# Optimization experiments

Measured on AMD Instinct MI355X. Metric: run time of the kernel, lower is better.

Reference implementation:

```python
import jax, jax.numpy as jnp
import numpy as np

B, T, C = 8, 2048, 1024   # batch, seq_len, n_embd
H = 128                   # head_size

def setup_inputs() -> dict:
    key = jax.random.key(0)
    kx, kk, kq, kv = jax.random.split(key, 4)
    scale = 1.0 / np.sqrt(C)
    return {
        "x": jax.random.normal(kx, (B, T, C), dtype=jnp.float32),
        "Wk": jax.random.normal(kk, (C, H), dtype=jnp.float32) * scale,
        "Wq": jax.random.normal(kq, (C, H), dtype=jnp.float32) * scale,
        "Wv": jax.random.normal(kv, (C, H), dtype=jnp.float32) * scale,
    }

def reference(x, Wk, Wq, Wv):
    # k,q,v: [B,T,H]
    k = x @ Wk
    q = x @ Wq
    v = x @ Wv
    # NOTE: original scales by C**-0.5 (n_embd), not head_size**-0.5
    wei = jnp.einsum("bth,bsh->bts", q, k) * (x.shape[-1] ** -0.5)  # [B,T,T]
    wei = jax.nn.softmax(wei, axis=-1)  # no causal mask in the source module
    # dropout = 0.0 -> identity
    out = jnp.einsum("bts,bsh->bth", wei, v)  # [B,T,H]
    return out
```

## Files before the change

kernel.cpp:

```cpp
#include <hip/hip_runtime.h>
#include <hip/hip_bf16.h>
#include <stdint.h>
#include <stddef.h>

#define NB 8
#define NT 2048
#define NC 1024
#define NH 128

typedef float f32x4 __attribute__((ext_vector_type(4)));
typedef short bf16x8 __attribute__((ext_vector_type(8)));

__device__ __forceinline__ unsigned short f2bf(float f) {
    union { float f; uint32_t u; } v; v.f = f;
    uint32_t u = v.u;
    u += 0x7fffu + ((u >> 16) & 1u);
    return (unsigned short)(u >> 16);
}

__device__ __forceinline__ void gld16(const void* gp, void* lp) {
    __builtin_amdgcn_global_load_lds(
        (const __attribute__((address_space(1))) unsigned int*)gp,
        (__attribute__((address_space(3))) unsigned int*)lp, 16, 0, 0);
}


__global__ __launch_bounds__(256) void cast_w_kernel(const float* __restrict__ Wq,
                                                     const float* __restrict__ Wk,
                                                     const float* __restrict__ Wv,
                                                     unsigned short* __restrict__ Wtf) {
    int gid  = blockIdx.x * 256 + threadIdx.x;
    int lane = gid & 63;
    int fs   = gid >> 6;
    int kb   = fs & 31;
    int g    = fs >> 5;
    int w    = g >> 3;
    int g16  = g & 7;
    int quad = lane >> 4;
    int l16  = lane & 15;
    const float* src = (w == 0) ? Wq : ((w == 1) ? Wk : Wv);
    int n = g16 * 16 + l16;
    bf16x8 o;
#pragma unroll
    for (int j = 0; j < 8; ++j)
        o[j] = (short)f2bf(src[(size_t)(kb * 32 + quad * 8 + j) * 128 + n]);
    *(bf16x8*)(Wtf + (size_t)gid * 8) = o;
}

#define CS2 392

__global__ __launch_bounds__(512, 2) void proj_kernel(const float* __restrict__ x,
                                                      const unsigned short* __restrict__ Wtf,
                                                      unsigned short* __restrict__ Qf,
                                                      unsigned short* __restrict__ Kf,
                                                      unsigned short* __restrict__ Vf) {
    __shared__ __align__(16) unsigned short wbuf[4][24 * 512];

    const int tid  = threadIdx.x;
    const int wave = tid >> 6;
    const int lane = tid & 63;
    const int quad = lane >> 4;
    const int l16  = lane & 15;
    const int bidx = blockIdx.x;
    const int rowbase = bidx * 64;
    const int b    = bidx >> 5;
    const int mh   = wave & 1;
    const int nq   = wave >> 1;

    const float* xr0 = x + (size_t)(rowbase + mh * 32 + l16) * NC;
    const float* xr1 = xr0 + (size_t)16 * NC;

    float4 aS[2][4];
    f32x4 acc0[6] = {};
    f32x4 acc1[6] = {};

#define STAGE(KB, BI) { _Pragma("unroll") \
    for (int i_ = 0; i_ < 3; ++i_) { \
        const int g_ = wave * 3 + i_; \
        gld16(Wtf + ((size_t)(g_ * 32 + (KB)) * 512) + lane * 8, &wbuf[BI][g_ * 512]); } }

#define LOADA(KB, S) { \
    const float* p0_ = xr0 + (KB) * 32 + quad * 8; \
    aS[S][0] = *(const float4*)p0_; \
    aS[S][1] = *(const float4*)(p0_ + 4); \
    const float* p1_ = xr1 + (KB) * 32 + quad * 8; \
    aS[S][2] = *(const float4*)p1_; \
    aS[S][3] = *(const float4*)(p1_ + 4); }

#define BARW(N) { asm volatile("s_waitcnt vmcnt(" #N ") lgkmcnt(0)" ::: "memory"); \
                  __builtin_amdgcn_s_barrier(); }

#define ITER(K, CUR, SLOT, DOA, DOST) { \
    bf16x8 af0, af1; \
    af0[0] = (short)f2bf(aS[SLOT][0].x); af0[1] = (short)f2bf(aS[SLOT][0].y); \
    af0[2] = (short)f2bf(aS[SLOT][0].z); af0[3] = (short)f2bf(aS[SLOT][0].w); \
    af0[4] = (short)f2bf(aS[SLOT][1].x); af0[5] = (short)f2bf(aS[SLOT][1].y); \
    af0[6] = (short)f2bf(aS[SLOT][1].z); af0[7] = (short)f2bf(aS[SLOT][1].w); \
    af1[0] = (short)f2bf(aS[SLOT][2].x); af1[1] = (short)f2bf(aS[SLOT][2].y); \
    af1[2] = (short)f2bf(aS[SLOT][2].z); af1[3] = (short)f2bf(aS[SLOT][2].w); \
    af1[4] = (short)f2bf(aS[SLOT][3].x); af1[5] = (short)f2bf(aS[SLOT][3].y); \
    af1[6] = (short)f2bf(aS[SLOT][3].z); af1[7] = (short)f2bf(aS[SLOT][3].w); \
    if (DOA)  LOADA((K) + 2, SLOT); \
    if (DOST) STAGE((K) + 3, ((K) + 3) & 3); \
    _Pragma("unroll") \
    for (int i_ = 0; i_ < 6; ++i_) { \
        bf16x8 wf_ = *(const bf16x8*)(&wbuf[CUR][(nq * 6 + i_) * 512 + lane * 8]); \
        acc0[i_] = __builtin_amdgcn_mfma_f32_16x16x32_bf16(af0, wf_, acc0[i_], 0, 0, 0); \
        acc1[i_] = __builtin_amdgcn_mfma_f32_16x16x32_bf16(af1, wf_, acc1[i_], 0, 0, 0); } }

    LOADA(0, 0); LOADA(1, 1);
    STAGE(0, 0); STAGE(1, 1); STAGE(2, 2);
    BARW(6);

    for (int kb4 = 0; kb4 < 28; kb4 += 4) {
        ITER(kb4 + 0, 0, 0, 1, 1); BARW(14);
        ITER(kb4 + 1, 1, 1, 1, 1); BARW(14);
        ITER(kb4 + 2, 2, 0, 1, 1); BARW(14);
        ITER(kb4 + 3, 3, 1, 1, 1); BARW(14);
    }
    ITER(28, 0, 0, 1, 1); BARW(14);
    ITER(29, 1, 1, 1, 0); BARW(11);
    ITER(30, 2, 0, 0, 0); BARW(4);
    ITER(31, 3, 1, 0, 0);
    asm volatile("s_waitcnt vmcnt(0) lgkmcnt(0)" ::: "memory");
    __builtin_amdgcn_s_barrier();

    unsigned short* cs = (unsigned short*)wbuf;
#pragma unroll
    for (int i = 0; i < 6; ++i) {
#pragma unroll
        for (int r = 0; r < 4; ++r) {
            cs[(mh * 32 +  0 + quad * 4 + r) * CS2 + nq * 96 + i * 16 + l16] = f2bf(acc0[i][r]);
            cs[(mh * 32 + 16 + quad * 4 + r) * CS2 + nq * 96 + i * 16 + l16] = f2bf(acc1[i][r]);
        }
    }
    __syncthreads();

    const int ibase = (rowbase & (NT - 1)) >> 4;
    const int tc    = (rowbase & (NT - 1)) >> 5;
    unsigned short* qdst = Qf + (size_t)b * (NT * NH);
    unsigned short* kdst = Kf + (size_t)b * (NT * NH);
    unsigned short* vdst = Vf + (size_t)b * (NT * NH);

#pragma unroll
    for (int j = 0; j < 6; ++j) {
        const int s = wave * 6 + j;
        if (s < 32) {
            const int isK = s >> 4;
            const int t   = s & 15;
            const int m   = t >> 2;
            const int ks  = t & 3;
            unsigned short* dst = isK ? kdst : qdst;
            bf16x8 v = *(const bf16x8*)(&cs[(m * 16 + l16) * CS2 + isK * 128 + ks * 32 + quad * 8]);
            *(bf16x8*)(dst + ((size_t)((ibase + m) * 4 + ks) * 64 + lane) * 8) = v;
        } else {
            const int vv = s - 32;
            const int nt = vv >> 1;
            const int cc = vv & 1;
            bf16x8 v;
#pragma unroll
            for (int jj = 0; jj < 8; ++jj)
                v[jj] = (short)cs[(cc * 32 + quad * 8 + jj) * CS2 + 256 + nt * 16 + l16];
            *(bf16x8*)(vdst + ((size_t)(nt * 64 + tc + cc) * 64 + lane) * 8) = v;
        }
    }

#undef ITER
#undef BARW
#undef LOADA
#undef STAGE
}

__global__ __launch_bounds__(256, 2) void attn_kernel(const unsigned short* __restrict__ Qf,
                                                      const unsigned short* __restrict__ Kf,
                                                      const unsigned short* __restrict__ Vf,
                                                      float* __restrict__ out) {
    __shared__ __align__(16) unsigned short kbuf[2][16 * 512];
    __shared__ __align__(16) unsigned short vbuf[2][16 * 512];
    __shared__ __align__(16) unsigned short p_all[4][16 * 40];
    __shared__ float sl[4][16];

    const int tid  = threadIdx.x;
    const int wave = tid >> 6;
    const int lane = tid & 63;
    const int quad = lane >> 4;
    const int l16  = lane & 15;
    const int bid  = blockIdx.x;
    const int b    = bid & 7;
    const int iqb  = bid >> 3;
    const int mt   = wave & 1;
    const int kh   = wave >> 1;
    const int iq   = iqb * 2 + mt;

    const unsigned short* qfp = Qf + (size_t)b * (NT * NH);
    const unsigned short* kfp = Kf + (size_t)b * (NT * NH);
    const unsigned short* vfp = Vf + (size_t)b * (NT * NH);
    unsigned short* p_w = p_all[wave];

    bf16x8 qf[4];
#pragma unroll
    for (int ks = 0; ks < 4; ++ks)
        qf[ks] = *(const bf16x8*)(qfp + ((size_t)(iq * 4 + ks) * 64 + lane) * 8);

    auto stage = [&](int j, int bi) {
#pragma unroll
        for (int i = 0; i < 8; ++i) {
            const int fid = wave * 8 + i;
            if (fid < 16) {
                gld16(kfp + ((size_t)(j * 16 + fid) * 512) + lane * 8, &kbuf[bi][fid * 512]);
            } else {
                const int s  = fid - 16;
                const int nt = s >> 1;
                const int c  = s & 1;
                gld16(vfp + ((size_t)(nt * 64 + j * 2 + c) * 512) + lane * 8, &vbuf[bi][s * 512]);
            }
        }
    };

    stage(0, 0);
    __syncthreads();

    f32x4 O[8] = {};
    float lsum[4] = {0.f, 0.f, 0.f, 0.f};
    const float scl2 = 0.03125f * 1.44269504088896340736f;

    for (int j = 0; j < 32; ++j) {
        const int cur = j & 1;
        if (j < 31) stage(j + 1, cur ^ 1);

        f32x4 S[2] = {};
#pragma unroll
        for (int ks = 0; ks < 4; ++ks) {
            bf16x8 kf0 = *(const bf16x8*)(&kbuf[cur][((kh * 2 + 0) * 4 + ks) * 512 + lane * 8]);
            bf16x8 kf1 = *(const bf16x8*)(&kbuf[cur][((kh * 2 + 1) * 4 + ks) * 512 + lane * 8]);
            S[0] = __builtin_amdgcn_mfma_f32_16x16x32_bf16(qf[ks], kf0, S[0], 0, 0, 0);
            S[1] = __builtin_amdgcn_mfma_f32_16x16x32_bf16(qf[ks], kf1, S[1], 0, 0, 0);
        }

#pragma unroll
        for (int n2 = 0; n2 < 2; ++n2) {
#pragma unroll
            for (int r = 0; r < 4; ++r) {
                float p = __builtin_amdgcn_exp2f(S[n2][r] * scl2);
                lsum[r] += p;
                p_w[(quad * 4 + r) * 40 + n2 * 16 + l16] = f2bf(p);
            }
        }

        bf16x8 pf = *(const bf16x8*)(&p_w[l16 * 40 + quad * 8]);
#pragma unroll
        for (int nt = 0; nt < 8; ++nt) {
            bf16x8 vf = *(const bf16x8*)(&vbuf[cur][(nt * 2 + kh) * 512 + lane * 8]);
            O[nt] = __builtin_amdgcn_mfma_f32_16x16x32_bf16(pf, vf, O[nt], 0, 0, 0);
        }

        __syncthreads();
    }

#pragma unroll
    for (int msk = 1; msk <= 8; msk <<= 1) {
#pragma unroll
        for (int r = 0; r < 4; ++r)
            lsum[r] += __shfl_xor(lsum[r], msk, 64);
    }

    if (l16 == 0) {
#pragma unroll
        for (int r = 0; r < 4; ++r)
            sl[wave][quad * 4 + r] = lsum[r];
    }
    float* so = (float*)kbuf;
    if (wave >= 2) {
#pragma unroll
        for (int nt = 0; nt < 8; ++nt) {
#pragma unroll
            for (int r = 0; r < 4; ++r)
                so[((size_t)(wave - 2) * 16 + quad * 4 + r) * 132 + nt * 16 + l16] = O[nt][r];
        }
    }
    __syncthreads();

    if (wave < 2) {
        float inv[4];
#pragma unroll
        for (int r = 0; r < 4; ++r)
            inv[r] = 1.0f / (sl[wave][quad * 4 + r] + sl[wave + 2][quad * 4 + r]);
        float* orow = out + ((size_t)b * NT + iq * 16) * NH;
#pragma unroll
        for (int nt = 0; nt < 8; ++nt) {
#pragma unroll
            for (int r = 0; r < 4; ++r) {
                float v = O[nt][r] + so[((size_t)wave * 16 + quad * 4 + r) * 132 + nt * 16 + l16];
                orow[(quad * 4 + r) * NH + nt * 16 + l16] = v * inv[r];
            }
        }
    }
}

extern "C" void kernel_launch(void* const* d_in, const int* in_sizes, int n_in,
                              void* d_out, int out_size, void* d_ws, size_t ws_size,
                              hipStream_t stream) {
    const float* x  = (const float*)d_in[0];
    const float* Wk = (const float*)d_in[1];
    const float* Wq = (const float*)d_in[2];
    const float* Wv = (const float*)d_in[3];
    float* out = (float*)d_out;

    char* ws = (char*)d_ws;
    unsigned short* Qf  = (unsigned short*)(ws);
    unsigned short* Kf  = (unsigned short*)(ws + 4194304);
    unsigned short* Vf  = (unsigned short*)(ws + 8388608);
    unsigned short* Wtf = (unsigned short*)(ws + 12582912);

    cast_w_kernel<<<192, 256, 0, stream>>>(Wq, Wk, Wv, Wtf);
    proj_kernel<<<256, 512, 0, stream>>>(x, Wtf, Qf, Kf, Vf);
    attn_kernel<<<512, 256, 0, stream>>>(Qf, Kf, Vf, out);
}
```

Measured before the change: 177.1 us.

## Stage x tiles through swizzled LDS with coalesced loads in projection kernel

The projection kernel's A operand (x rows) is now read in coalesced 128-float chunks per row. Each chunk is converted to bf16 once and written into a double-buffered, XOR-swizzled LDS tile. MFMA fragments are then read from LDS instead of converting per-lane strided global loads every k-step. The pipeline schedule is rewritten with new vmcnt waits, and the extra 32KB of LDS may reduce occupancy.

```diff
diff --git a/kernel.cpp b/kernel.cpp
--- a/kernel.cpp
+++ b/kernel.cpp
@@ -10,6 +10,7 @@
 
 typedef float f32x4 __attribute__((ext_vector_type(4)));
 typedef short bf16x8 __attribute__((ext_vector_type(8)));
+typedef short bf16x4 __attribute__((ext_vector_type(4)));
 
 __device__ __forceinline__ unsigned short f2bf(float f) {
     union { float f; uint32_t u; } v; v.f = f;
@@ -55,6 +56,7 @@
                                                       unsigned short* __restrict__ Kf,
                                                       unsigned short* __restrict__ Vf) {
     __shared__ __align__(16) unsigned short wbuf[4][24 * 512];
+    __shared__ __align__(16) unsigned short abuf[2][64 * 128];
 
     const int tid  = threadIdx.x;
     const int wave = tid >> 6;
@@ -67,8 +69,10 @@
     const int mh   = wave & 1;
     const int nq   = wave >> 1;
 
-    const float* xr0 = x + (size_t)(rowbase + mh * 32 + l16) * NC;
-    const float* xr1 = xr0 + (size_t)16 * NC;
+    const int arow = wave * 8 + (lane >> 3);
+    const float* axp = x + (size_t)(rowbase + arow) * NC;
+    const int aswz = (arow & 7) << 3;
+    const int rswz = (l16 & 7) << 3;
 
     float4 aS[2][4];
     f32x4 acc0[6] = {};
@@ -79,29 +83,25 @@
         const int g_ = wave * 3 + i_; \
         gld16(Wtf + ((size_t)(g_ * 32 + (KB)) * 512) + lane * 8, &wbuf[BI][g_ * 512]); } }
 
-#define LOADA(KB, S) { \
-    const float* p0_ = xr0 + (KB) * 32 + quad * 8; \
-    aS[S][0] = *(const float4*)p0_; \
-    aS[S][1] = *(const float4*)(p0_ + 4); \
-    const float* p1_ = xr1 + (KB) * 32 + quad * 8; \
-    aS[S][2] = *(const float4*)p1_; \
-    aS[S][3] = *(const float4*)(p1_ + 4); }
+#define LOADA(C, S) { _Pragma("unroll") \
+    for (int i_ = 0; i_ < 4; ++i_) \
+        aS[S][i_] = *(const float4*)(axp + (C) * 128 + i_ * 32 + (lane & 7) * 4); }
+
+#define DSWRITE(C, S) { _Pragma("unroll") \
+    for (int i_ = 0; i_ < 4; ++i_) { \
+        bf16x4 t_; \
+        t_[0] = (short)f2bf(aS[S][i_].x); t_[1] = (short)f2bf(aS[S][i_].y); \
+        t_[2] = (short)f2bf(aS[S][i_].z); t_[3] = (short)f2bf(aS[S][i_].w); \
+        *(bf16x4*)(&abuf[(C) & 1][arow * 128 + ((i_ * 32 + (lane & 7) * 4) ^ aswz)]) = t_; } }
 
 #define BARW(N) { asm volatile("s_waitcnt vmcnt(" #N ") lgkmcnt(0)" ::: "memory"); \
                   __builtin_amdgcn_s_barrier(); }
 
-#define ITER(K, CUR, SLOT, DOA, DOST) { \
-    bf16x8 af0, af1; \
-    af0[0] = (short)f2bf(aS[SLOT][0].x); af0[1] = (short)f2bf(aS[SLOT][0].y); \
-    af0[2] = (short)f2bf(aS[SLOT][0].z); af0[3] = (short)f2bf(aS[SLOT][0].w); \
-    af0[4] = (short)f2bf(aS[SLOT][1].x); af0[5] = (short)f2bf(aS[SLOT][1].y); \
-    af0[6] = (short)f2bf(aS[SLOT][1].z); af0[7] = (short)f2bf(aS[SLOT][1].w); \
-    af1[0] = (short)f2bf(aS[SLOT][2].x); af1[1] = (short)f2bf(aS[SLOT][2].y); \
-    af1[2] = (short)f2bf(aS[SLOT][2].z); af1[3] = (short)f2bf(aS[SLOT][2].w); \
-    af1[4] = (short)f2bf(aS[SLOT][3].x); af1[5] = (short)f2bf(aS[SLOT][3].y); \
-    af1[6] = (short)f2bf(aS[SLOT][3].z); af1[7] = (short)f2bf(aS[SLOT][3].w); \
-    if (DOA)  LOADA((K) + 2, SLOT); \
-    if (DOST) STAGE((K) + 3, ((K) + 3) & 3); \
+#define TICK(K, CUR) { \
+    const unsigned short* ab_ = abuf[((K) >> 2) & 1]; \
+    const int t2_ = ((K) & 3) * 32 + quad * 8; \
+    bf16x8 af0 = *(const bf16x8*)(ab_ + (mh * 32 + l16) * 128 + (t2_ ^ rswz)); \
+    bf16x8 af1 = *(const bf16x8*)(ab_ + (mh * 32 + 16 + l16) * 128 + (t2_ ^ rswz)); \
     _Pragma("unroll") \
     for (int i_ = 0; i_ < 6; ++i_) { \
         bf16x8 wf_ = *(const bf16x8*)(&wbuf[CUR][(nq * 6 + i_) * 512 + lane * 8]); \
@@ -110,18 +110,26 @@
 
     LOADA(0, 0); LOADA(1, 1);
     STAGE(0, 0); STAGE(1, 1); STAGE(2, 2);
+    asm volatile("s_waitcnt vmcnt(13)" ::: "memory");
+    DSWRITE(0, 0);
     BARW(6);
 
-    for (int kb4 = 0; kb4 < 28; kb4 += 4) {
-        ITER(kb4 + 0, 0, 0, 1, 1); BARW(14);
-        ITER(kb4 + 1, 1, 1, 1, 1); BARW(14);
-        ITER(kb4 + 2, 2, 0, 1, 1); BARW(14);
-        ITER(kb4 + 3, 3, 1, 1, 1); BARW(14);
-    }
-    ITER(28, 0, 0, 1, 1); BARW(14);
-    ITER(29, 1, 1, 1, 0); BARW(11);
-    ITER(30, 2, 0, 0, 0); BARW(4);
-    ITER(31, 3, 1, 0, 0);
+    for (int c = 0; c < 6; ++c) {
+        const int k0 = c * 4;
+        LOADA(c + 2, c & 1);
+        STAGE(k0 + 3, 3); TICK(k0 + 0, 0); BARW(10);
+        STAGE(k0 + 4, 0); TICK(k0 + 1, 1); BARW(10);
+        STAGE(k0 + 5, 1); TICK(k0 + 2, 2); BARW(6);
+        STAGE(k0 + 6, 2); TICK(k0 + 3, 3); DSWRITE(c + 1, (c + 1) & 1); BARW(6);
+    }
+    STAGE(27, 3); TICK(24, 0); BARW(6);
+    STAGE(28, 0); TICK(25, 1); BARW(6);
+    STAGE(29, 1); TICK(26, 2); BARW(6);
+    STAGE(30, 2); TICK(27, 3); DSWRITE(7, 1); BARW(6);
+    STAGE(31, 3); TICK(28, 0); BARW(6);
+    TICK(29, 1); BARW(3);
+    TICK(30, 2); BARW(0);
+    TICK(31, 3);
     asm volatile("s_waitcnt vmcnt(0) lgkmcnt(0)" ::: "memory");
     __builtin_amdgcn_s_barrier();
 
@@ -165,8 +173,9 @@
         }
     }
 
-#undef ITER
+#undef TICK
 #undef BARW
+#undef DSWRITE
 #undef LOADA
 #undef STAGE
 }
```

New measurement: 158.9 us. 1.11x faster.
